# Optimization experiments

Hardware: AMD Instinct MI355X
Metric: run time of the kernel (lower is better)

The kernel has to match this reference:

```python
import jax, jax.numpy as jnp
import numpy as np


def _next_pow2(n: int) -> int:
    return 1 << (int(n) - 1).bit_length()


def setup_inputs() -> dict:
    key = jax.random.key(0)
    k1, k2 = jax.random.split(key)
    B, T, L = 256, 65536, 65536  # batch, seq_len, filter length (L >= T so epoched recurrence == full causal conv)
    x = jax.random.normal(k1, (B, T), dtype=jnp.float32)
    filt = jax.random.normal(k2, (1, L), dtype=jnp.float32) / np.float32(np.sqrt(L))
    return {"x": x, "filt": filt}


def reference(x, filt):
    """EpochedFutureFill.forward == causal FIR convolution of x with filt.

    The torch module's per-token loop (sliced dot-product + FFT-refreshed
    FutureFill cache every K steps) computes exactly
        y[:, t] = sum_{s=0}^{t} filt[0, s] * x[:, t - s]
    for t < T <= L. We express that directly as one FFT convolution,
    mirroring the module's own future_fill (pow-2 rfft/irfft) math.
    """
    B, T = x.shape
    L = filt.shape[-1]
    n_fft = _next_pow2(T + L - 1)
    xf = jnp.fft.rfft(x, n=n_fft)        # (B, n_fft//2+1) complex
    ff = jnp.fft.rfft(filt, n=n_fft)     # (1, n_fft//2+1) complex, broadcasts over batch
    y_full = jnp.fft.irfft(xf * ff, n=n_fft)
    return y_full[:, :T]                 # causal part: (B, T)
```

## Files before the change

kernel.cpp:

```cpp
#include <hip/hip_runtime.h>


#define N_FFT 131072
#define N1    512
#define N2    256
#define T_LEN 65536
#define CB    128
#define PI_F  3.14159265358979323846f
#define R2_F  0.70710678118654752f
#define C16F  0.92387953251128675613f
#define S16F  0.38268343236508977173f

typedef __attribute__((ext_vector_type(2))) __fp16 h2;
typedef __attribute__((ext_vector_type(4))) __fp16 h4;
typedef __attribute__((ext_vector_type(8))) __fp16 h8;

__device__ inline int brev9(int x) { return (int)(__brev((unsigned)x) >> 23); }

__device__ inline float2 cadd(float2 a, float2 b){ return make_float2(a.x+b.x, a.y+b.y); }
__device__ inline float2 csub(float2 a, float2 b){ return make_float2(a.x-b.x, a.y-b.y); }
__device__ inline float2 cmul(float2 a, float2 b){ return make_float2(a.x*b.x-a.y*b.y, a.x*b.y+a.y*b.x); }
__device__ inline float2 cmulc(float2 a, float2 b){ return make_float2(a.x*b.x+a.y*b.y, a.y*b.x-a.x*b.y); }
__device__ inline float2 csq(float2 a){ return make_float2(a.x*a.x-a.y*a.y, 2.f*a.x*a.y); }
__device__ inline float2 conjf(float2 a){ return make_float2(a.x, -a.y); }
__device__ inline float2 expif(float a){ float s,c; __sincosf(a,&s,&c); return make_float2(c,s); }
__device__ inline h2 f2h(float2 v){ return __builtin_amdgcn_cvt_pkrtz(v.x, v.y); }

__device__ inline float2 mul_mi(float2 a){ return make_float2(a.y, -a.x); }
__device__ inline float2 mul_pi(float2 a){ return make_float2(-a.y, a.x); }
__device__ inline float2 mul_w81(float2 a){ return make_float2(R2_F*(a.x+a.y), R2_F*(a.y-a.x)); }
__device__ inline float2 mul_w83(float2 a){ return make_float2(R2_F*(a.y-a.x), -R2_F*(a.x+a.y)); }
__device__ inline float2 mul_w81c(float2 a){ return make_float2(R2_F*(a.x-a.y), R2_F*(a.x+a.y)); }
__device__ inline float2 mul_w83c(float2 a){ return make_float2(-R2_F*(a.x+a.y), R2_F*(a.x-a.y)); }

__device__ inline void dif4(float2&a0, float2&a1, float2&a2, float2&a3, float2 w1, float2 w2){
    float2 s02 = cadd(a0,a2), d02 = csub(a0,a2);
    float2 s13 = cadd(a1,a3), d13 = csub(a1,a3);
    float2 b2 = cmul(w1,d02);
    float2 t  = cmul(w1,d13);
    float2 b3 = make_float2(t.y, -t.x);
    a0 = cadd(s02,s13);
    a1 = cmul(w2, csub(s02,s13));
    a2 = cadd(b2,b3);
    a3 = cmul(w2, csub(b2,b3));
}

__device__ inline void dit4i(float2&a0, float2&a1, float2&a2, float2&a3, float2 w1, float2 w2){
    float2 t1 = cmul(w1,a1), t3 = cmul(w1,a3);
    float2 u0 = cadd(a0,t1), u1 = csub(a0,t1);
    float2 u2 = cadd(a2,t3), u3 = csub(a2,t3);
    float2 s2 = cmul(w2,u2), s3 = cmul(w2,u3);
    a0 = cadd(u0,s2); a2 = csub(u0,s2);
    a1 = make_float2(u1.x - s3.y, u1.y + s3.x);
    a3 = make_float2(u1.x + s3.y, u1.y - s3.x);
}

__device__ constexpr int BR[16] = {0,8,4,12,2,10,6,14,1,9,5,13,3,11,7,15};

__device__ __forceinline__ void fft16_fwd(float2 v[16]){
    {
        float2 s02=cadd(v[0],v[8]),  d02=csub(v[0],v[8]);
        float2 s13=cadd(v[4],v[12]), d13=csub(v[4],v[12]);
        float2 b3 = mul_mi(d13);
        v[0]=cadd(s02,s13); v[4]=csub(s02,s13);
        v[8]=cadd(d02,b3);  v[12]=csub(d02,b3);
    }
    {
        float2 s02=cadd(v[1],v[9]),  d02=csub(v[1],v[9]);
        float2 s13=cadd(v[5],v[13]), d13=csub(v[5],v[13]);
        const float2 w1 = make_float2(C16F,-S16F);
        float2 b2 = cmul(w1,d02), b3 = mul_mi(cmul(w1,d13));
        v[1]=cadd(s02,s13);  v[5]=mul_w81(csub(s02,s13));
        v[9]=cadd(b2,b3);    v[13]=mul_w81(csub(b2,b3));
    }
    {
        float2 s02=cadd(v[2],v[10]), d02=csub(v[2],v[10]);
        float2 s13=cadd(v[6],v[14]), d13=csub(v[6],v[14]);
        float2 b2 = mul_w81(d02), b3 = mul_mi(mul_w81(d13));
        v[2]=cadd(s02,s13);  v[6]=mul_mi(csub(s02,s13));
        v[10]=cadd(b2,b3);   v[14]=mul_mi(csub(b2,b3));
    }
    {
        float2 s02=cadd(v[3],v[11]), d02=csub(v[3],v[11]);
        float2 s13=cadd(v[7],v[15]), d13=csub(v[7],v[15]);
        const float2 w1 = make_float2(S16F,-C16F);
        float2 b2 = cmul(w1,d02), b3 = mul_mi(cmul(w1,d13));
        v[3]=cadd(s02,s13);  v[7]=mul_w83(csub(s02,s13));
        v[11]=cadd(b2,b3);   v[15]=mul_w83(csub(b2,b3));
    }
#pragma unroll
    for (int q=0;q<4;q++){
        float2 a0=v[4*q],a1=v[4*q+1],a2=v[4*q+2],a3=v[4*q+3];
        float2 s02=cadd(a0,a2), d02=csub(a0,a2);
        float2 s13=cadd(a1,a3), d13=csub(a1,a3);
        float2 b3 = mul_mi(d13);
        v[4*q]=cadd(s02,s13);   v[4*q+1]=csub(s02,s13);
        v[4*q+2]=cadd(d02,b3);  v[4*q+3]=csub(d02,b3);
    }
}

__device__ __forceinline__ void fft16_inv(float2 v[16]){
#pragma unroll
    for (int q=0;q<4;q++){
        float2 a0=v[4*q],a1=v[4*q+1],a2=v[4*q+2],a3=v[4*q+3];
        float2 u0=cadd(a0,a1), u1=csub(a0,a1);
        float2 u2=cadd(a2,a3), u3=csub(a2,a3);
        v[4*q]=cadd(u0,u2);   v[4*q+2]=csub(u0,u2);
        v[4*q+1]=make_float2(u1.x-u3.y, u1.y+u3.x);
        v[4*q+3]=make_float2(u1.x+u3.y, u1.y-u3.x);
    }
    {
        float2 t1=v[4], t3=v[12];
        float2 u0=cadd(v[0],t1), u1=csub(v[0],t1);
        float2 u2=cadd(v[8],t3), u3=csub(v[8],t3);
        v[0]=cadd(u0,u2); v[8]=csub(u0,u2);
        v[4]=make_float2(u1.x-u3.y, u1.y+u3.x);
        v[12]=make_float2(u1.x+u3.y, u1.y-u3.x);
    }
    {
        float2 t1=mul_w81c(v[5]), t3=mul_w81c(v[13]);
        float2 u0=cadd(v[1],t1), u1=csub(v[1],t1);
        float2 u2=cadd(v[9],t3), u3=csub(v[9],t3);
        const float2 w2 = make_float2(C16F,S16F);
        float2 s2=cmul(w2,u2), s3=cmul(w2,u3);
        v[1]=cadd(u0,s2); v[9]=csub(u0,s2);
        v[5]=make_float2(u1.x-s3.y, u1.y+s3.x);
        v[13]=make_float2(u1.x+s3.y, u1.y-s3.x);
    }
    {
        float2 t1=mul_pi(v[6]), t3=mul_pi(v[14]);
        float2 u0=cadd(v[2],t1), u1=csub(v[2],t1);
        float2 u2=cadd(v[10],t3), u3=csub(v[10],t3);
        float2 s2=mul_w81c(u2), s3=mul_w81c(u3);
        v[2]=cadd(u0,s2); v[10]=csub(u0,s2);
        v[6]=make_float2(u1.x-s3.y, u1.y+s3.x);
        v[14]=make_float2(u1.x+s3.y, u1.y-s3.x);
    }
    {
        float2 t1=mul_w83c(v[7]), t3=mul_w83c(v[15]);
        float2 u0=cadd(v[3],t1), u1=csub(v[3],t1);
        float2 u2=cadd(v[11],t3), u3=csub(v[11],t3);
        const float2 w2 = make_float2(S16F,C16F);
        float2 s2=cmul(w2,u2), s3=cmul(w2,u3);
        v[3]=cadd(u0,s2); v[11]=csub(u0,s2);
        v[7]=make_float2(u1.x-s3.y, u1.y+s3.x);
        v[15]=make_float2(u1.x+s3.y, u1.y-s3.x);
    }
}

template<bool HALF>
__global__ __launch_bounds__(512, 4) void fwd_cols(
    const float* __restrict__ re_base, const float* __restrict__ im_base,
    long long row_stride, void* __restrict__ dstv)
{
    __shared__ float2 s[N1 * 16];
    const int tile = blockIdx.x, row = blockIdx.y, tid = threadIdx.x;
    const int n2base = tile * 16;
    const float* rp = re_base + (long long)row * row_stride;
    const float* ip = im_base ? (im_base + (long long)row * row_stride) : nullptr;

    {
        const int cp = tid & 7, n1g = tid >> 3;
#pragma unroll
        for (int i = 0; i < 4; i++) {
            int n1 = n1g + 64 * i;
            int g  = n1 * N2 + n2base + 2 * cp;
            float2 a = *(const float2*)(rp + g);
            float2 b = ip ? *(const float2*)(ip + g) : make_float2(0.f, 0.f);
            s[n1 * 16 + 2 * cp]     = make_float2(a.x, b.x);
            s[n1 * 16 + 2 * cp + 1] = make_float2(a.y, b.y);
        }
    }
    __syncthreads();

    const int c = tid & 15, r = tid >> 4;

    {
        float2 w1 = expif((float)r * (-PI_F / 256.f));
        const float2 stp = make_float2(0.92387953251f, -0.38268343236f);
#pragma unroll
        for (int qq = 0; qq < 4; qq++) {
            int j = r + 32 * qq;
            float2 w2 = csq(w1);
            float2 a0 = s[j * 16 + c], a1 = s[(j + 128) * 16 + c];
            float2 b2 = cmul(w1, a0);
            float2 t  = cmul(w1, a1);
            float2 b3 = make_float2(t.y, -t.x);
            s[j * 16 + c]         = cadd(a0, a1);
            s[(j + 128) * 16 + c] = cmul(w2, csub(a0, a1));
            s[(j + 256) * 16 + c] = cadd(b2, b3);
            s[(j + 384) * 16 + c] = cmul(w2, csub(b2, b3));
            w1 = cmul(w1, stp);
        }
    }
    __syncthreads();

    {
        float2 w1 = expif((float)r * (-PI_F / 64.f));
        float2 w2 = csq(w1);
#pragma unroll
        for (int qq = 0; qq < 4; qq++) {
            int p0 = qq * 128 + r;
            float2 a0 = s[p0*16+c], a1 = s[(p0+32)*16+c], a2 = s[(p0+64)*16+c], a3 = s[(p0+96)*16+c];
            dif4(a0, a1, a2, a3, w1, w2);
            s[p0*16+c] = a0; s[(p0+32)*16+c] = a1; s[(p0+64)*16+c] = a2; s[(p0+96)*16+c] = a3;
        }
    }
    __syncthreads();

    {
        float2 w1 = expif((float)(r & 7) * (-PI_F / 16.f));
        float2 w2 = csq(w1);
#pragma unroll
        for (int qq = 0; qq < 4; qq++) {
            int g = (r >> 3) + 4 * qq;
            int p0 = g * 32 + (r & 7);
            float2 a0 = s[p0*16+c], a1 = s[(p0+8)*16+c], a2 = s[(p0+16)*16+c], a3 = s[(p0+24)*16+c];
            dif4(a0, a1, a2, a3, w1, w2);
            s[p0*16+c] = a0; s[(p0+8)*16+c] = a1; s[(p0+16)*16+c] = a2; s[(p0+24)*16+c] = a3;
        }
    }
    __syncthreads();

    const int n2 = n2base + c;
    const float2 w1c = make_float2(R2_F, -R2_F);
    const float2 w2c = make_float2(0.f, -1.f);
    const float2 one = make_float2(1.f, 0.f);
    const float2 w64 = expif((float)n2 * (-PI_F / 1024.f));
#pragma unroll
    for (int o = 0; o < 2; o++) {
        int base = 8 * (r + 32 * o);
        float2 v[8];
#pragma unroll
        for (int m = 0; m < 8; m++) v[m] = s[(base + m) * 16 + c];
        dif4(v[0], v[2], v[4], v[6], one, one);
        dif4(v[1], v[3], v[5], v[7], w1c, w2c);
#pragma unroll
        for (int m = 0; m < 8; m += 2) {
            float2 a = v[m], b = v[m + 1];
            v[m] = cadd(a, b); v[m + 1] = csub(a, b);
        }
        const int Kb = brev9(base);
        float2 wK = expif((float)(n2 * Kb) * (-2.f * PI_F / (float)N_FFT));
        float2 pw[8];
        pw[0] = one;
#pragma unroll
        for (int k = 1; k < 8; k++) pw[k] = cmul(pw[k-1], w64);
        const int b3tab[8] = {0,4,2,6,1,5,3,7};
#pragma unroll
        for (int m = 0; m < 8; m++) {
            int b  = b3tab[m];
            int k1 = Kb + 64 * b;
            float2 w = cmul(wK, pw[b]);
            float2 rv = cmul(v[m], w);
            if (HALF) {
                h2* drow = (h2*)dstv + (size_t)row * N_FFT;
                drow[(size_t)k1 * N2 + n2] = f2h(rv);
            } else {
                float2* drow = (float2*)dstv + (size_t)row * N_FFT;
                drow[(size_t)k1 * N2 + n2] = rv;
            }
        }
    }
}

#define RPITCH 18

__global__ __launch_bounds__(128) void fwd_rows_g(float2* __restrict__ G)
{
    __shared__ __align__(16) float2 s[8 * 16 * RPITCH + 16 * RPITCH];
    const int tid = threadIdx.x;
    const int t = tid & 15, rl = tid >> 4;
    const long long row = (long long)blockIdx.x * 8 + rl;
    float2* tab = s + 8 * 16 * RPITCH;

    {
        int b0 = tid >> 4, c0 = tid & 15;
        tab[b0 * RPITCH + c0] = expif((float)(b0 * c0) * (-2.f * PI_F / 256.f));
        int e = tid + 128, b1 = e >> 4, c1 = e & 15;
        tab[b1 * RPITCH + c1] = expif((float)(b1 * c1) * (-2.f * PI_F / 256.f));
    }
    __syncthreads();

    const float2* gp = G + (size_t)row * N2 + t;
    float2 v[16];
#pragma unroll
    for (int a = 0; a < 16; a++) v[a] = gp[16 * a];

    fft16_fwd(v);
#pragma unroll
    for (int p = 1; p < 16; p++) v[p] = cmul(v[p], tab[t * RPITCH + BR[p]]);

    float2* rS = s + rl * (16 * RPITCH);
    float4* rS4 = (float4*)rS;
#pragma unroll
    for (int k = 0; k < 8; k++) {
        float2 e = v[BR[2*k]], o = v[BR[2*k] + 8];
        rS4[(t * RPITCH + 2*k) >> 1] = make_float4(e.x, e.y, o.x, o.y);
    }
    asm volatile("s_waitcnt lgkmcnt(0)" ::: "memory");
#pragma unroll
    for (int b = 0; b < 16; b++) v[b] = rS[b * RPITCH + t];

    fft16_fwd(v);

    float4* o4 = (float4*)(G + (size_t)row * N2 + 16 * t);
#pragma unroll
    for (int m = 0; m < 8; m++)
        o4[m] = make_float4(v[2*m].x, v[2*m].y, v[2*m+1].x, v[2*m+1].y);
}

__global__ __launch_bounds__(256, 4) void mid_rows(
    h2* __restrict__ buf, const float2* __restrict__ Gh)
{
    __shared__ __align__(16) float2 s[16 * 16 * RPITCH + 16 * RPITCH];
    const int tid = threadIdx.x;
    const int t = tid & 15, rl = tid >> 4;
    const long long row = (long long)blockIdx.x * 16 + rl;
    const int k1 = (int)(row & (N1 - 1));
    float2* tab = s + 16 * 16 * RPITCH;

    {
        int b = tid >> 4, c = tid & 15;
        tab[b * RPITCH + c] = expif((float)(b * c) * (-2.f * PI_F / 256.f));
    }
    __syncthreads();

    h2* bp = buf + ((size_t)row * N2 + t);
    float2 v[16];
#pragma unroll
    for (int a = 0; a < 16; a++) {
        h2 h = bp[16 * a];
        v[a] = make_float2((float)h.x, (float)h.y);
    }

    fft16_fwd(v);
#pragma unroll
    for (int p = 1; p < 16; p++) v[p] = cmul(v[p], tab[t * RPITCH + BR[p]]);

    float2* rS = s + rl * (16 * RPITCH);
    float4* rS4 = (float4*)rS;
#pragma unroll
    for (int k = 0; k < 8; k++) {
        float2 e = v[BR[2*k]], o = v[BR[2*k] + 8];
        rS4[(t * RPITCH + 2*k) >> 1] = make_float4(e.x, e.y, o.x, o.y);
    }

    const float4* g4 = (const float4*)(Gh + ((size_t)k1 * N2 + 16 * t));
    float4 g[8];
#pragma unroll
    for (int m = 0; m < 8; m++) g[m] = g4[m];

    asm volatile("s_waitcnt lgkmcnt(0)" ::: "memory");
#pragma unroll
    for (int b = 0; b < 16; b++) v[b] = rS[b * RPITCH + t];

    fft16_fwd(v);

#pragma unroll
    for (int m = 0; m < 8; m++) {
        v[2*m]   = cmul(v[2*m],   make_float2(g[m].x, g[m].y));
        v[2*m+1] = cmul(v[2*m+1], make_float2(g[m].z, g[m].w));
    }

    fft16_inv(v);
#pragma unroll
    for (int b = 1; b < 16; b++) v[b] = cmulc(v[b], tab[b * RPITCH + t]);

#pragma unroll
    for (int m = 0; m < 8; m++)
        rS4[(t * RPITCH + 2*m) >> 1] = make_float4(v[2*m].x, v[2*m].y, v[2*m+1].x, v[2*m+1].y);
    asm volatile("s_waitcnt lgkmcnt(0)" ::: "memory");
#pragma unroll
    for (int c = 0; c < 16; c++) v[BR[c]] = rS[c * RPITCH + t];

    fft16_inv(v);

    {
        const float th = 2.f * PI_F / (float)N_FFT;
        float2 w = expif((float)(k1 * t) * th);
        const float2 stp = expif((float)(16 * k1) * th);
#pragma unroll
        for (int a = 0; a < 16; a++) {
            float2 r = cmul(v[a], w);
            bp[16 * a] = f2h(r);
            if (a < 15) w = cmul(w, stp);
        }
    }
}

__global__ __launch_bounds__(512, 4) void inv_cols(
    const h2* __restrict__ src, float* __restrict__ out)
{
    __shared__ float4 s4[N1 * 16 / 2];
    float2* s = (float2*)s4;
    const int tile = blockIdx.x, row = blockIdx.y, tid = threadIdx.x;
    const int n2base = tile * 16;
    const h2* srow = src + (size_t)row * N_FFT;
    const int cp = tid & 7, r8 = tid >> 3;

#pragma unroll
    for (int i = 0; i < 8; i++) {
        int k1 = r8 + 64 * i;
        h4 v = *((const h4*)(srow + (size_t)k1 * N2 + n2base + 2 * cp));
        int p = brev9(k1);
        s4[p * 8 + cp] = make_float4((float)v.x, (float)v.y, (float)v.z, (float)v.w);
    }
    __syncthreads();

    const int c = tid & 15, r = tid >> 4;

    const float2 w1c = make_float2(0.f, 1.f);
    const float2 w2c = make_float2(R2_F, R2_F);
    const float2 one = make_float2(1.f, 0.f);
#pragma unroll
    for (int o = 0; o < 2; o++) {
        int base = 8 * (r + 32 * o);
        float2 v[8];
#pragma unroll
        for (int m = 0; m < 8; m++) v[m] = s[(base + m) * 16 + c];
#pragma unroll
        for (int m = 0; m < 8; m += 2) {
            float2 a = v[m], b = v[m + 1];
            v[m] = cadd(a, b); v[m + 1] = csub(a, b);
        }
        dit4i(v[0], v[2], v[4], v[6], one, one);
        dit4i(v[1], v[3], v[5], v[7], w1c, w2c);
#pragma unroll
        for (int m = 0; m < 8; m++) s[(base + m) * 16 + c] = v[m];
    }
    __syncthreads();

    {
        float2 w2 = expif((float)(r & 7) * (PI_F / 16.f));
        float2 w1 = csq(w2);
#pragma unroll
        for (int qq = 0; qq < 4; qq++) {
            int g = (r >> 3) + 4 * qq;
            int p0 = g * 32 + (r & 7);
            float2 a0 = s[p0*16+c], a1 = s[(p0+8)*16+c], a2 = s[(p0+16)*16+c], a3 = s[(p0+24)*16+c];
            dit4i(a0, a1, a2, a3, w1, w2);
            s[p0*16+c] = a0; s[(p0+8)*16+c] = a1; s[(p0+16)*16+c] = a2; s[(p0+24)*16+c] = a3;
        }
    }
    __syncthreads();
    {
        float2 w2 = expif((float)r * (PI_F / 64.f));
        float2 w1 = csq(w2);
#pragma unroll
        for (int qq = 0; qq < 4; qq++) {
            int p0 = qq * 128 + r;
            float2 a0 = s[p0*16+c], a1 = s[(p0+32)*16+c], a2 = s[(p0+64)*16+c], a3 = s[(p0+96)*16+c];
            dit4i(a0, a1, a2, a3, w1, w2);
            s[p0*16+c] = a0; s[(p0+32)*16+c] = a1; s[(p0+64)*16+c] = a2; s[(p0+96)*16+c] = a3;
        }
    }
    __syncthreads();
    {
        float2 w2 = expif((float)r * (PI_F / 256.f));
        const float2 stp = make_float2(0.92387953251f, 0.38268343236f);
#pragma unroll
        for (int qq = 0; qq < 4; qq++) {
            int j = r + 32 * qq;
            float2 w1 = csq(w2);
            float2 a0 = s[j*16+c], a1 = s[(j+128)*16+c], a2 = s[(j+256)*16+c], a3 = s[(j+384)*16+c];
            dit4i(a0, a1, a2, a3, w1, w2);
            s[j*16+c] = a0; s[(j+128)*16+c] = a1; s[(j+256)*16+c] = a2; s[(j+384)*16+c] = a3;
            w2 = cmul(w2, stp);
        }
    }
    __syncthreads();

    const float scale = 1.0f / (float)N_FFT;
    float* out0 = out + (size_t)(2 * row) * T_LEN;
    float* out1 = out + (size_t)(2 * row + 1) * T_LEN;
#pragma unroll
    for (int i = 0; i < 4; i++) {
        int p = r8 + 64 * i;
        float4 q = s4[p * 8 + cp];
        int n = p * N2 + n2base + 2 * cp;
        *(float2*)(out0 + n) = make_float2(q.x * scale, q.z * scale);
        *(float2*)(out1 + n) = make_float2(q.y * scale, q.w * scale);
    }
}

extern "C" void kernel_launch(void* const* d_in, const int* in_sizes, int n_in,
                              void* d_out, int out_size, void* d_ws, size_t ws_size,
                              hipStream_t stream) {
    const float* x    = (const float*)d_in[0];
    const float* filt = (const float*)d_in[1];
    float* out = (float*)d_out;

    h2* buf = (h2*)d_ws;
    float2* G = (float2*)((char*)d_ws + (size_t)CB * N_FFT * sizeof(h2));

    fwd_cols<false><<<dim3(16, 1), 512, 0, stream>>>(filt, nullptr, 0LL, (void*)G);
    fwd_rows_g<<<N1 / 8, 128, 0, stream>>>(G);
    fwd_cols<true><<<dim3(16, CB), 512, 0, stream>>>(x, x + T_LEN, (long long)(2 * T_LEN), (void*)buf);
    mid_rows<<<(CB * N1) / 16, 256, 0, stream>>>(buf, G);
    inv_cols<<<dim3(16, CB), 512, 0, stream>>>(buf, out);
}
```

Baseline: 220.4 us.

## Restructure forward column FFT as register radix-16 x radix-32 with one shared transpose

Rewrites the forward column-FFT kernel so each thread loads 8 strided inputs into registers and runs a zero-padded radix-16 FFT there. It then applies twiddles from a small shared table and does a single shared-memory transpose, followed by a radix-2 split and a second radix-16 FFT in registers. This replaces the previous four-pass shared-memory radix-4 pipeline with several barriers. Tiles shrink to 8 columns with 256 threads, doubling the grid. The aim is less shared-memory traffic and fewer syncs, at the cost of higher register pressure and narrower per-thread global loads.

```diff
diff --git a/kernel.cpp b/kernel.cpp
--- a/kernel.cpp
+++ b/kernel.cpp
@@ -99,6 +99,44 @@
     }
 }
 
+__device__ __forceinline__ void fft16_fwd_z8(float2 v[16]){
+    {
+        float2 a=v[0], b=v[4];
+        float2 ib = mul_mi(b);
+        v[0]=cadd(a,b); v[4]=csub(a,b);
+        v[8]=cadd(a,ib); v[12]=csub(a,ib);
+    }
+    {
+        float2 a=v[1], b=v[5];
+        const float2 w1 = make_float2(C16F,-S16F);
+        float2 wa = cmul(w1,a), wb = mul_mi(cmul(w1,b));
+        v[1]=cadd(a,b);   v[5]=mul_w81(csub(a,b));
+        v[9]=cadd(wa,wb); v[13]=mul_w81(csub(wa,wb));
+    }
+    {
+        float2 a=v[2], b=v[6];
+        float2 wa = mul_w81(a), wb = mul_mi(mul_w81(b));
+        v[2]=cadd(a,b);    v[6]=mul_mi(csub(a,b));
+        v[10]=cadd(wa,wb); v[14]=mul_mi(csub(wa,wb));
+    }
+    {
+        float2 a=v[3], b=v[7];
+        const float2 w1 = make_float2(S16F,-C16F);
+        float2 wa = cmul(w1,a), wb = mul_mi(cmul(w1,b));
+        v[3]=cadd(a,b);    v[7]=mul_w83(csub(a,b));
+        v[11]=cadd(wa,wb); v[15]=mul_w83(csub(wa,wb));
+    }
+#pragma unroll
+    for (int q=0;q<4;q++){
+        float2 a0=v[4*q],a1=v[4*q+1],a2=v[4*q+2],a3=v[4*q+3];
+        float2 s02=cadd(a0,a2), d02=csub(a0,a2);
+        float2 s13=cadd(a1,a3), d13=csub(a1,a3);
+        float2 b3 = mul_mi(d13);
+        v[4*q]=cadd(s02,s13);   v[4*q+1]=csub(s02,s13);
+        v[4*q+2]=cadd(d02,b3);  v[4*q+3]=csub(d02,b3);
+    }
+}
+
 __device__ __forceinline__ void fft16_inv(float2 v[16]){
 #pragma unroll
     for (int q=0;q<4;q++){
@@ -148,119 +186,104 @@
     }
 }
 
+#define XPC 34
+#define XPN 546
+
 template<bool HALF>
-__global__ __launch_bounds__(512, 4) void fwd_cols(
+__global__ __launch_bounds__(256, 4) void fwd_cols(
     const float* __restrict__ re_base, const float* __restrict__ im_base,
     long long row_stride, void* __restrict__ dstv)
 {
-    __shared__ float2 s[N1 * 16];
-    const int tile = blockIdx.x, row = blockIdx.y, tid = threadIdx.x;
-    const int n2base = tile * 16;
+    __shared__ __align__(16) float2 s[8 * XPN + 32 * 17];
+    const int tid = threadIdx.x;
+    const int tile = blockIdx.x, row = blockIdx.y;
+    const int n2base = tile * 8;
+    float2* tab = s + 8 * XPN;
+
+    {
+        int q = tid >> 4, c = tid & 15;
+        tab[q * 17 + c]        = expif((float)(q * c) * (-2.f * PI_F / 512.f));
+        tab[(q + 16) * 17 + c] = expif((float)((q + 16) * c) * (-2.f * PI_F / 512.f));
+    }
+    __syncthreads();
+
+    const int n2l = tid & 7, q = tid >> 3;
     const float* rp = re_base + (long long)row * row_stride;
     const float* ip = im_base ? (im_base + (long long)row * row_stride) : nullptr;
 
-    {
-        const int cp = tid & 7, n1g = tid >> 3;
-#pragma unroll
-        for (int i = 0; i < 4; i++) {
-            int n1 = n1g + 64 * i;
-            int g  = n1 * N2 + n2base + 2 * cp;
-            float2 a = *(const float2*)(rp + g);
-            float2 b = ip ? *(const float2*)(ip + g) : make_float2(0.f, 0.f);
-            s[n1 * 16 + 2 * cp]     = make_float2(a.x, b.x);
-            s[n1 * 16 + 2 * cp + 1] = make_float2(a.y, b.y);
-        }
-    }
-    __syncthreads();
-
-    const int c = tid & 15, r = tid >> 4;
-
-    {
-        float2 w1 = expif((float)r * (-PI_F / 256.f));
-        const float2 stp = make_float2(0.92387953251f, -0.38268343236f);
-#pragma unroll
-        for (int qq = 0; qq < 4; qq++) {
-            int j = r + 32 * qq;
-            float2 w2 = csq(w1);
-            float2 a0 = s[j * 16 + c], a1 = s[(j + 128) * 16 + c];
-            float2 b2 = cmul(w1, a0);
-            float2 t  = cmul(w1, a1);
-            float2 b3 = make_float2(t.y, -t.x);
-            s[j * 16 + c]         = cadd(a0, a1);
-            s[(j + 128) * 16 + c] = cmul(w2, csub(a0, a1));
-            s[(j + 256) * 16 + c] = cadd(b2, b3);
-            s[(j + 384) * 16 + c] = cmul(w2, csub(b2, b3));
-            w1 = cmul(w1, stp);
-        }
-    }
-    __syncthreads();
-
-    {
-        float2 w1 = expif((float)r * (-PI_F / 64.f));
-        float2 w2 = csq(w1);
-#pragma unroll
-        for (int qq = 0; qq < 4; qq++) {
-            int p0 = qq * 128 + r;
-            float2 a0 = s[p0*16+c], a1 = s[(p0+32)*16+c], a2 = s[(p0+64)*16+c], a3 = s[(p0+96)*16+c];
-            dif4(a0, a1, a2, a3, w1, w2);
-            s[p0*16+c] = a0; s[(p0+32)*16+c] = a1; s[(p0+64)*16+c] = a2; s[(p0+96)*16+c] = a3;
-        }
-    }
-    __syncthreads();
-
-    {
-        float2 w1 = expif((float)(r & 7) * (-PI_F / 16.f));
-        float2 w2 = csq(w1);
-#pragma unroll
-        for (int qq = 0; qq < 4; qq++) {
-            int g = (r >> 3) + 4 * qq;
-            int p0 = g * 32 + (r & 7);
-            float2 a0 = s[p0*16+c], a1 = s[(p0+8)*16+c], a2 = s[(p0+16)*16+c], a3 = s[(p0+24)*16+c];
-            dif4(a0, a1, a2, a3, w1, w2);
-            s[p0*16+c] = a0; s[(p0+8)*16+c] = a1; s[(p0+16)*16+c] = a2; s[(p0+24)*16+c] = a3;
-        }
-    }
-    __syncthreads();
-
-    const int n2 = n2base + c;
-    const float2 w1c = make_float2(R2_F, -R2_F);
-    const float2 w2c = make_float2(0.f, -1.f);
-    const float2 one = make_float2(1.f, 0.f);
-    const float2 w64 = expif((float)n2 * (-PI_F / 1024.f));
-#pragma unroll
-    for (int o = 0; o < 2; o++) {
-        int base = 8 * (r + 32 * o);
-        float2 v[8];
-#pragma unroll
-        for (int m = 0; m < 8; m++) v[m] = s[(base + m) * 16 + c];
-        dif4(v[0], v[2], v[4], v[6], one, one);
-        dif4(v[1], v[3], v[5], v[7], w1c, w2c);
-#pragma unroll
-        for (int m = 0; m < 8; m += 2) {
-            float2 a = v[m], b = v[m + 1];
-            v[m] = cadd(a, b); v[m + 1] = csub(a, b);
-        }
-        const int Kb = brev9(base);
-        float2 wK = expif((float)(n2 * Kb) * (-2.f * PI_F / (float)N_FFT));
-        float2 pw[8];
-        pw[0] = one;
-#pragma unroll
-        for (int k = 1; k < 8; k++) pw[k] = cmul(pw[k-1], w64);
-        const int b3tab[8] = {0,4,2,6,1,5,3,7};
-#pragma unroll
-        for (int m = 0; m < 8; m++) {
-            int b  = b3tab[m];
-            int k1 = Kb + 64 * b;
-            float2 w = cmul(wK, pw[b]);
-            float2 rv = cmul(v[m], w);
-            if (HALF) {
-                h2* drow = (h2*)dstv + (size_t)row * N_FFT;
-                drow[(size_t)k1 * N2 + n2] = f2h(rv);
-            } else {
-                float2* drow = (float2*)dstv + (size_t)row * N_FFT;
-                drow[(size_t)k1 * N2 + n2] = rv;
-            }
-        }
+    float2 v[16];
+    if (ip) {
+#pragma unroll
+        for (int p = 0; p < 8; p++) {
+            int g = (32 * p + q) * N2 + n2base + n2l;
+            v[p] = make_float2(rp[g], ip[g]);
+        }
+    } else {
+#pragma unroll
+        for (int p = 0; p < 8; p++) {
+            int g = (32 * p + q) * N2 + n2base + n2l;
+            v[p] = make_float2(rp[g], 0.f);
+        }
+    }
+    fft16_fwd_z8(v);
+
+#pragma unroll
+    for (int c = 1; c < 16; c++) v[BR[c]] = cmul(v[BR[c]], tab[q * 17 + c]);
+#pragma unroll
+    for (int c = 0; c < 16; c++) s[n2l * XPN + c * XPC + q] = v[BR[c]];
+    __syncthreads();
+
+    const int sI = tid >> 3;
+    const int cc = sI & 15, jj = sI >> 4;
+    const float4* z4 = (const float4*)(s + n2l * XPN + cc * XPC);
+    float2 b[16];
+    if (jj == 0) {
+#pragma unroll
+        for (int k = 0; k < 8; k++) {
+            float4 A = z4[k], B = z4[k + 8];
+            b[2*k]   = make_float2(A.x + B.x, A.y + B.y);
+            b[2*k+1] = make_float2(A.z + B.z, A.w + B.w);
+        }
+    } else {
+        constexpr float CT[16] = {
+            1.f, 0.98078528040323044913f, 0.92387953251128675613f, 0.83146961230254523708f,
+            0.70710678118654752440f, 0.55557023301960222474f, 0.38268343236508977173f,
+            0.19509032201612826785f, 0.f, -0.19509032201612826785f, -0.38268343236508977173f,
+            -0.55557023301960222474f, -0.70710678118654752440f, -0.83146961230254523708f,
+            -0.92387953251128675613f, -0.98078528040323044913f };
+        constexpr float ST[16] = {
+            0.f, -0.19509032201612826785f, -0.38268343236508977173f, -0.55557023301960222474f,
+            -0.70710678118654752440f, -0.83146961230254523708f, -0.92387953251128675613f,
+            -0.98078528040323044913f, -1.f, -0.98078528040323044913f, -0.92387953251128675613f,
+            -0.83146961230254523708f, -0.70710678118654752440f, -0.55557023301960222474f,
+            -0.38268343236508977173f, -0.19509032201612826785f };
+#pragma unroll
+        for (int k = 0; k < 8; k++) {
+            float4 A = z4[k], B = z4[k + 8];
+            float2 d0 = make_float2(A.x - B.x, A.y - B.y);
+            float2 d1 = make_float2(A.z - B.z, A.w - B.w);
+            b[2*k]   = (k == 0) ? d0 : cmul(d0, make_float2(CT[2*k], ST[2*k]));
+            b[2*k+1] = cmul(d1, make_float2(CT[2*k+1], ST[2*k+1]));
+        }
+    }
+    fft16_fwd(b);
+
+    const int n2 = n2base + n2l;
+    const float th = -2.f * PI_F / (float)N_FFT;
+    float2 w   = expif(th * (float)(n2 * (cc + 16 * jj)));
+    float2 stp = expif(th * (float)(32 * n2));
+#pragma unroll
+    for (int m = 0; m < 16; m++) {
+        float2 rv = cmul(b[BR[m]], w);
+        int k1 = cc + 32 * m + 16 * jj;
+        if (HALF) {
+            h2* drow = (h2*)dstv + (size_t)row * N_FFT;
+            drow[(size_t)k1 * N2 + n2] = f2h(rv);
+        } else {
+            float2* drow = (float2*)dstv + (size_t)row * N_FFT;
+            drow[(size_t)k1 * N2 + n2] = rv;
+        }
+        if (m < 15) w = cmul(w, stp);
     }
 }
 
@@ -494,9 +517,9 @@
     h2* buf = (h2*)d_ws;
     float2* G = (float2*)((char*)d_ws + (size_t)CB * N_FFT * sizeof(h2));
 
-    fwd_cols<false><<<dim3(16, 1), 512, 0, stream>>>(filt, nullptr, 0LL, (void*)G);
+    fwd_cols<false><<<dim3(32, 1), 256, 0, stream>>>(filt, nullptr, 0LL, (void*)G);
     fwd_rows_g<<<N1 / 8, 128, 0, stream>>>(G);
-    fwd_cols<true><<<dim3(16, CB), 512, 0, stream>>>(x, x + T_LEN, (long long)(2 * T_LEN), (void*)buf);
+    fwd_cols<true><<<dim3(32, CB), 256, 0, stream>>>(x, x + T_LEN, (long long)(2 * T_LEN), (void*)buf);
     mid_rows<<<(CB * N1) / 16, 256, 0, stream>>>(buf, G);
     inv_cols<<<dim3(16, CB), 512, 0, stream>>>(buf, out);
 }
```

New measurement: 244.1 us. 1.11x slower.
